# Optimization experiments

Measured on AMD Instinct MI355X. Metric: run time of the kernel, lower is better.

The kernel has to match this reference:

```python
import jax, jax.numpy as jnp
import numpy as np

DECAY = 0.9
BETA_OBS = 1.0
BETA_STATE = 1.0

N_OBS = 20000
N_STATES = 1024
N_ACTIONS = 64
STATE_DIM = 256
RFD = 2048


def setup_inputs() -> dict:
    key = jax.random.key(0)
    ks = jax.random.split(key, 7)
    Q = jax.random.normal(ks[0], (STATE_DIM, N_STATES), dtype=jnp.float32) / np.sqrt(STATE_DIM).astype(np.float32)
    V = jax.random.normal(ks[1], (STATE_DIM, N_ACTIONS), dtype=jnp.float32) / np.sqrt(STATE_DIM).astype(np.float32)
    W = jax.random.normal(ks[2], (RFD, STATE_DIM), dtype=jnp.float32)
    M_re = jax.random.normal(ks[3], (RFD, N_OBS), dtype=jnp.float32)
    M_im = jax.random.normal(ks[4], (RFD, N_OBS), dtype=jnp.float32)
    obs = jax.random.uniform(ks[5], (N_OBS,), dtype=jnp.float32)
    action = jax.random.uniform(ks[6], (N_ACTIONS,), dtype=jnp.float32)
    return {"Q": Q, "V": V, "W": W, "M_re": M_re, "M_im": M_im, "obs": obs, "action": action}


def reference(Q, V, W, M_re, M_im, obs, action):
    # One fused POCML step: memory write (decayed outer product), state
    # rotation via complex random-feature phase, clean_up (state-kernel
    # softmax retrieval), and obs retrieval from memory.
    D = W.shape[0]  # random_feature_dim
    M = M_re + 1j * M_im                       # [D, n_obs] complex64
    obs_c = obs.astype(jnp.complex64)
    # get_state_from_memory
    state0 = M @ obs_c                         # [D]
    # update_memory: M *= decay; M += outer(state, obs)
    M_new = DECAY * M + jnp.outer(state0, obs_c)
    # update_state: v = V @ action; phi_v = exp(1j * W @ v); state *= phi_v
    v = V @ action                             # [state_dim]
    phi_v = jnp.exp(1j * (W @ v))              # [D] complex64
    state1 = state0 * phi_v
    # clean_up: phi_Q = exp(1j * W @ Q), weights = softmax(beta*sim(phi_Q.T, state))
    phi_Q = jnp.exp(1j * (W @ Q))              # [D, n_states]
    score = BETA_STATE * (phi_Q.T @ jnp.conj(state1)).real / D  # [n_states]
    weights = jax.nn.softmax(score)
    state2 = phi_Q @ weights.astype(jnp.complex64)              # [D]
    # get_obs_from_memory: softmax(beta_obs * sim(M.T, state))
    obs_score = BETA_OBS * (M_new.T @ jnp.conj(state2)).real / D  # [n_obs]
    return jax.nn.softmax(obs_score)
```

## Files before the change

### kernel.cpp

```cpp
#include <hip/hip_runtime.h>
#include <math.h>

#define N_OBS    20000
#define N_OBS4   5000
#define N_STATES 1024
#define N_ACT    64
#define SDIM     256
#define RFD      2048
#define DECAY    0.9f

typedef float v4f __attribute__((ext_vector_type(4)));

__device__ __forceinline__ v4f ld4(const float* p) {
    return *(const v4f*)p;
}
__device__ __forceinline__ v4f ntload4(const float* p) {
    return __builtin_nontemporal_load((const v4f*)p);
}

#define OFF_SCORE  0
#define OFF_OBSACC 1024
#define ZERO_CNT   (OFF_OBSACC + N_OBS)
#define OFF_S0RE   21024
#define OFF_S0IM   23072
#define OFF_S2RE   25120
#define OFF_S2IM   27168
#define OFF_WTS    29216
#define OFF_VWS    30240
#define OFF_COSQ   30496
#define OFF_SINQ   (OFF_COSQ + RFD*N_STATES)
#define WS_FLOATS  (OFF_SINQ + RFD*N_STATES)

#define NB_GEMM   512
#define NB_P1     RFD
#define NB_FUSED  (NB_GEMM + 1 + NB_P1)

__global__ __launch_bounds__(256) void k_fused(
    const float* __restrict__ Mre, const float* __restrict__ Mim,
    const float* __restrict__ obs,
    const float* __restrict__ W, const float* __restrict__ Q,
    const float* __restrict__ V, const float* __restrict__ action,
    float* __restrict__ cosQ, float* __restrict__ sinQ,
    float* __restrict__ s0re, float* __restrict__ s0im,
    float* __restrict__ vout)
{
    const int b = blockIdx.x;
    const int tid = threadIdx.x;

    if (b < NB_GEMM) {
        __shared__ float As[16][65];
        __shared__ float Bs[16][64];
        const int tx = tid & 15;
        const int ty = tid >> 4;
        const int m0 = (b >> 4) * 64;
        const int n0 = (b & 15) * 64;
        float c[4][4] = {};
        for (int k0 = 0; k0 < SDIM; k0 += 16) {
            {
                int k = tid & 15, mb = tid >> 4;
                #pragma unroll
                for (int j = 0; j < 4; j++)
                    As[k][mb + 16*j] = W[(size_t)(m0 + mb + 16*j) * SDIM + k0 + k];
            }
            {
                int n = tid & 63, kb = tid >> 6;
                #pragma unroll
                for (int j = 0; j < 4; j++)
                    Bs[kb + 4*j][n] = Q[(size_t)(k0 + kb + 4*j) * N_STATES + n0 + n];
            }
            __syncthreads();
            #pragma unroll
            for (int kk = 0; kk < 16; kk++) {
                float a[4], bb[4];
                #pragma unroll
                for (int i = 0; i < 4; i++) a[i] = As[kk][ty*4 + i];
                #pragma unroll
                for (int j = 0; j < 4; j++) bb[j] = Bs[kk][tx*4 + j];
                #pragma unroll
                for (int i = 0; i < 4; i++)
                    #pragma unroll
                    for (int j = 0; j < 4; j++)
                        c[i][j] += a[i] * bb[j];
            }
            __syncthreads();
        }
        #pragma unroll
        for (int i = 0; i < 4; i++) {
            int d = m0 + ty*4 + i;
            #pragma unroll
            for (int j = 0; j < 4; j++) {
                int s = n0 + tx*4 + j;
                float sn, cs;
                sincosf(c[i][j], &sn, &cs);
                cosQ[(size_t)d * N_STATES + s] = cs;
                sinQ[(size_t)d * N_STATES + s] = sn;
            }
        }
    } else if (b == NB_GEMM) {
        float acc = 0.f;
        for (int a = 0; a < N_ACT; a++) acc += V[tid * N_ACT + a] * action[a];
        vout[tid] = acc;
    } else {
        const int d = b - (NB_GEMM + 1);
        const float* mr = Mre + (size_t)d * N_OBS;
        const float* mi = Mim + (size_t)d * N_OBS;
        const float4* ob = (const float4*)obs;
        float ar[4] = {0.f, 0.f, 0.f, 0.f}, ai[4] = {0.f, 0.f, 0.f, 0.f};
        int i = tid;
        #pragma unroll 4
        for (int it = 0; it < 19; ++it, i += 256) {
            float4 o = ob[i];
            v4f a = ld4(mr + 4 * (size_t)i);
            v4f m = ld4(mi + 4 * (size_t)i);
            ar[it & 3] += a.x*o.x + a.y*o.y + a.z*o.z + a.w*o.w;
            ai[it & 3] += m.x*o.x + m.y*o.y + m.z*o.z + m.w*o.w;
        }
        if (i < N_OBS4) {
            float4 o = ob[i];
            v4f a = ld4(mr + 4 * (size_t)i);
            v4f m = ld4(mi + 4 * (size_t)i);
            ar[3] += a.x*o.x + a.y*o.y + a.z*o.z + a.w*o.w;
            ai[3] += m.x*o.x + m.y*o.y + m.z*o.z + m.w*o.w;
        }
        float arr = (ar[0] + ar[1]) + (ar[2] + ar[3]);
        float aii = (ai[0] + ai[1]) + (ai[2] + ai[3]);
        #pragma unroll
        for (int off = 32; off > 0; off >>= 1) {
            arr += __shfl_down(arr, off);
            aii += __shfl_down(aii, off);
        }
        __shared__ float pr[4], pi[4];
        const int wave = tid >> 6, lane = tid & 63;
        if (lane == 0) { pr[wave] = arr; pi[wave] = aii; }
        __syncthreads();
        if (tid == 0) {
            s0re[d] = pr[0] + pr[1] + pr[2] + pr[3];
            s0im[d] = pi[0] + pi[1] + pi[2] + pi[3];
        }
    }
}

__global__ __launch_bounds__(256) void k_score(
    const float* __restrict__ cosQ, const float* __restrict__ sinQ,
    const float* __restrict__ W, const float* __restrict__ vws,
    const float* __restrict__ s0re, const float* __restrict__ s0im,
    float* __restrict__ score)
{
    __shared__ float s1r_s[32], s1i_s[32];
    const int tid = threadIdx.x;
    const int d0 = blockIdx.y * 32;
    {
        const int r = tid >> 3, g = tid & 7;
        const float4* wv4 = (const float4*)(W + (size_t)(d0 + r) * SDIM + g * 32);
        const float4* vv4 = (const float4*)(vws + g * 32);
        float th = 0.f;
        #pragma unroll
        for (int j = 0; j < 8; j++) {
            float4 wv = wv4[j], vv = vv4[j];
            th += wv.x*vv.x + wv.y*vv.y + wv.z*vv.z + wv.w*vv.w;
        }
        th += __shfl_xor(th, 4);
        th += __shfl_xor(th, 2);
        th += __shfl_xor(th, 1);
        if (g == 0) {
            float sn, cs;
            sincosf(th, &sn, &cs);
            float re = s0re[d0 + r], im = s0im[d0 + r];
            s1r_s[r] = re * cs - im * sn;
            s1i_s[r] = re * sn + im * cs;
        }
    }
    __syncthreads();
    const int s = blockIdx.x * 256 + tid;
    float acc = 0.f;
    #pragma unroll 4
    for (int j = 0; j < 32; j++) {
        int d = d0 + j;
        acc += cosQ[(size_t)d * N_STATES + s] * s1r_s[j]
             + sinQ[(size_t)d * N_STATES + s] * s1i_s[j];
    }
    atomicAdd(&score[s], acc);
}

__global__ __launch_bounds__(256) void k_softmax_w(
    const float* __restrict__ score, float* __restrict__ wts)
{
    __shared__ float red[256];
    const int tid = threadIdx.x;
    const float scale = 1.f / (float)RFD;
    float4 v = ((const float4*)score)[tid];
    v.x *= scale; v.y *= scale; v.z *= scale; v.w *= scale;
    float mx = fmaxf(fmaxf(v.x, v.y), fmaxf(v.z, v.w));
    red[tid] = mx; __syncthreads();
    for (int s = 128; s > 0; s >>= 1) {
        if (tid < s) red[tid] = fmaxf(red[tid], red[tid+s]);
        __syncthreads();
    }
    mx = red[0]; __syncthreads();
    float4 e;
    e.x = expf(v.x - mx); e.y = expf(v.y - mx);
    e.z = expf(v.z - mx); e.w = expf(v.w - mx);
    red[tid] = e.x + e.y + e.z + e.w; __syncthreads();
    for (int s = 128; s > 0; s >>= 1) {
        if (tid < s) red[tid] += red[tid+s];
        __syncthreads();
    }
    const float inv = 1.f / red[0];
    e.x *= inv; e.y *= inv; e.z *= inv; e.w *= inv;
    ((float4*)wts)[tid] = e;
}

__global__ __launch_bounds__(256) void k_state2(
    const float* __restrict__ cosQ, const float* __restrict__ sinQ,
    const float* __restrict__ wts,
    float* __restrict__ s2re, float* __restrict__ s2im)
{
    __shared__ float r1[256], r2[256];
    const int d = blockIdx.x, tid = threadIdx.x;
    float4 w = ((const float4*)wts)[tid];
    float4 a = ((const float4*)(cosQ + (size_t)d * N_STATES))[tid];
    float4 b = ((const float4*)(sinQ + (size_t)d * N_STATES))[tid];
    r1[tid] = a.x*w.x + a.y*w.y + a.z*w.z + a.w*w.w;
    r2[tid] = b.x*w.x + b.y*w.y + b.z*w.z + b.w*w.w;
    __syncthreads();
    for (int s = 128; s > 0; s >>= 1) {
        if (tid < s) { r1[tid] += r1[tid+s]; r2[tid] += r2[tid+s]; }
        __syncthreads();
    }
    if (tid == 0) { s2re[d] = r1[0]; s2im[d] = r2[0]; }
}

__global__ __launch_bounds__(256) void k_obs_acc(
    const float* __restrict__ Mre, const float* __restrict__ Mim,
    const float* __restrict__ s2re, const float* __restrict__ s2im,
    float* __restrict__ obs_acc)
{
    __shared__ float c_s[64], s_s[64];
    const int tid = threadIdx.x;
    const int dbase = (31 - (int)blockIdx.y) * 64;
    if (tid < 64) { c_s[tid] = s2re[dbase + tid]; s_s[tid] = s2im[dbase + tid]; }
    __syncthreads();
    const int idx = blockIdx.x * 256 + tid;
    if (idx >= N_OBS4) return;
    float4 acc[4];
    #pragma unroll
    for (int u = 0; u < 4; u++) acc[u] = make_float4(0.f, 0.f, 0.f, 0.f);
    #pragma unroll 8
    for (int j = 0; j < 64; j++) {
        size_t base = ((size_t)(dbase + j) * N_OBS4 + idx) * 4;
        v4f a = ntload4(Mre + base);
        v4f b = ntload4(Mim + base);
        float cc = c_s[j], ss = s_s[j];
        acc[j & 3].x += a.x*cc + b.x*ss;
        acc[j & 3].y += a.y*cc + b.y*ss;
        acc[j & 3].z += a.z*cc + b.z*ss;
        acc[j & 3].w += a.w*cc + b.w*ss;
    }
    float4 t;
    t.x = (acc[0].x + acc[1].x) + (acc[2].x + acc[3].x);
    t.y = (acc[0].y + acc[1].y) + (acc[2].y + acc[3].y);
    t.z = (acc[0].z + acc[1].z) + (acc[2].z + acc[3].z);
    t.w = (acc[0].w + acc[1].w) + (acc[2].w + acc[3].w);
    atomicAdd(&obs_acc[idx*4 + 0], t.x);
    atomicAdd(&obs_acc[idx*4 + 1], t.y);
    atomicAdd(&obs_acc[idx*4 + 2], t.z);
    atomicAdd(&obs_acc[idx*4 + 3], t.w);
}

__global__ __launch_bounds__(1024) void k_softmax_obs(
    const float* __restrict__ obs_acc, const float* __restrict__ obs,
    const float* __restrict__ s0re, const float* __restrict__ s0im,
    const float* __restrict__ s2re, const float* __restrict__ s2im,
    float* __restrict__ out)
{
    __shared__ float red[1024];
    const int tid = threadIdx.x;
    float dp = 0.f;
    #pragma unroll
    for (int i = 0; i < 2; i++) {
        int d = tid + i * 1024;
        dp += s0re[d] * s2re[d] + s0im[d] * s2im[d];
    }
    red[tid] = dp; __syncthreads();
    for (int s = 512; s > 0; s >>= 1) {
        if (tid < s) red[tid] += red[tid+s];
        __syncthreads();
    }
    const float d0 = red[0];
    __syncthreads();
    const float scale = 1.f / (float)RFD;
    float vals[20];
    float mx = -3.402823466e+38f;
    #pragma unroll
    for (int i = 0; i < 20; i++) {
        int idx = tid + i * 1024;
        if (idx < N_OBS) {
            float sc = (DECAY * obs_acc[idx] + obs[idx] * d0) * scale;
            vals[i] = sc;
            mx = fmaxf(mx, sc);
        } else vals[i] = -3.402823466e+38f;
    }
    red[tid] = mx; __syncthreads();
    for (int s = 512; s > 0; s >>= 1) {
        if (tid < s) red[tid] = fmaxf(red[tid], red[tid+s]);
        __syncthreads();
    }
    mx = red[0]; __syncthreads();
    float sum = 0.f;
    #pragma unroll
    for (int i = 0; i < 20; i++) {
        int idx = tid + i * 1024;
        if (idx < N_OBS) {
            vals[i] = expf(vals[i] - mx);
            sum += vals[i];
        }
    }
    red[tid] = sum; __syncthreads();
    for (int s = 512; s > 0; s >>= 1) {
        if (tid < s) red[tid] += red[tid+s];
        __syncthreads();
    }
    const float inv = 1.f / red[0];
    #pragma unroll
    for (int i = 0; i < 20; i++) {
        int idx = tid + i * 1024;
        if (idx < N_OBS) out[idx] = vals[i] * inv;
    }
}

extern "C" void kernel_launch(void* const* d_in, const int* in_sizes, int n_in,
                              void* d_out, int out_size, void* d_ws, size_t ws_size,
                              hipStream_t stream) {
    const float* Q      = (const float*)d_in[0];
    const float* V      = (const float*)d_in[1];
    const float* W      = (const float*)d_in[2];
    const float* Mre    = (const float*)d_in[3];
    const float* Mim    = (const float*)d_in[4];
    const float* obs    = (const float*)d_in[5];
    const float* action = (const float*)d_in[6];
    float* out = (float*)d_out;
    float* ws  = (float*)d_ws;

    if (ws_size < (size_t)WS_FLOATS * sizeof(float)) return;

    float* score = ws + OFF_SCORE;
    float* oacc  = ws + OFF_OBSACC;
    float* s0re  = ws + OFF_S0RE;
    float* s0im  = ws + OFF_S0IM;
    float* s2re  = ws + OFF_S2RE;
    float* s2im  = ws + OFF_S2IM;
    float* wts   = ws + OFF_WTS;
    float* vws   = ws + OFF_VWS;
    float* cosQ  = ws + OFF_COSQ;
    float* sinQ  = ws + OFF_SINQ;

    hipMemsetAsync(ws, 0, (size_t)ZERO_CNT * sizeof(float), stream);

    k_fused<<<NB_FUSED, 256, 0, stream>>>(Mre, Mim, obs, W, Q, V, action,
                                          cosQ, sinQ, s0re, s0im, vws);
    k_score<<<dim3(4, 64), 256, 0, stream>>>(cosQ, sinQ, W, vws, s0re, s0im, score);
    k_softmax_w<<<1, 256, 0, stream>>>(score, wts);
    k_state2<<<RFD, 256, 0, stream>>>(cosQ, sinQ, wts, s2re, s2im);
    k_obs_acc<<<dim3(20, 32), 256, 0, stream>>>(Mre, Mim, s2re, s2im, oacc);
    k_softmax_obs<<<1, 1024, 0, stream>>>(oacc, obs, s0re, s0im, s2re, s2im, out);
}
```

Before: 421.8 us.

## Stash fp16 interleaved copy of memory matrix for second pass

During the first pass over M_re/M_im (computing state0), blocks now handle two rows each and also write an interleaved fp16 copy of M into workspace. The later obs-score pass reads this half-size copy instead of re-reading both fp32 matrices, halving its traffic. The cost is extra write traffic in the first pass, fp16 rounding of M in the obs scores, and reliance on a much larger workspace, with a fallback to the fp32 path when the workspace is too small. Block ordering in the fused kernel and the obs pass is also changed.

```diff
diff --git a/kernel.cpp b/kernel.cpp
--- a/kernel.cpp
+++ b/kernel.cpp
@@ -1,4 +1,5 @@
 #include <hip/hip_runtime.h>
+#include <hip/hip_fp16.h>
 #include <math.h>
 
 #define N_OBS    20000
@@ -16,6 +17,15 @@
 }
 __device__ __forceinline__ v4f ntload4(const float* p) {
     return __builtin_nontemporal_load((const v4f*)p);
+}
+
+__device__ __forceinline__ uint4 pack8(v4f re, v4f im) {
+    union { __half h[8]; uint4 u; } p;
+    p.h[0] = __float2half_rn(re.x); p.h[1] = __float2half_rn(im.x);
+    p.h[2] = __float2half_rn(re.y); p.h[3] = __float2half_rn(im.y);
+    p.h[4] = __float2half_rn(re.z); p.h[5] = __float2half_rn(im.z);
+    p.h[6] = __float2half_rn(re.w); p.h[7] = __float2half_rn(im.w);
+    return p.u;
 }
 
 #define OFF_SCORE  0
@@ -29,11 +39,14 @@
 #define OFF_VWS    30240
 #define OFF_COSQ   30496
 #define OFF_SINQ   (OFF_COSQ + RFD*N_STATES)
-#define WS_FLOATS  (OFF_SINQ + RFD*N_STATES)
-
+#define OFF_MH     (OFF_SINQ + RFD*N_STATES)
+#define MH_FLOATS  (RFD * N_OBS4 * 4)
+#define WS_BASE_FLOATS (OFF_MH)
+#define WS_FP16_FLOATS (OFF_MH + MH_FLOATS)
+
+#define NB_P1     (RFD / 2)
 #define NB_GEMM   512
-#define NB_P1     RFD
-#define NB_FUSED  (NB_GEMM + 1 + NB_P1)
+#define NB_FUSED  (NB_P1 + 1 + NB_GEMM)
 
 __global__ __launch_bounds__(256) void k_fused(
     const float* __restrict__ Mre, const float* __restrict__ Mim,
@@ -42,18 +55,116 @@
     const float* __restrict__ V, const float* __restrict__ action,
     float* __restrict__ cosQ, float* __restrict__ sinQ,
     float* __restrict__ s0re, float* __restrict__ s0im,
-    float* __restrict__ vout)
+    float* __restrict__ vout, uint4* __restrict__ Mh, int writeMh)
 {
     const int b = blockIdx.x;
     const int tid = threadIdx.x;
 
-    if (b < NB_GEMM) {
+    if (b < NB_P1) {
+        const int d0 = b * 2;
+        const float* mr0 = Mre + (size_t)d0 * N_OBS;
+        const float* mi0 = Mim + (size_t)d0 * N_OBS;
+        const float* mr1 = mr0 + N_OBS;
+        const float* mi1 = mi0 + N_OBS;
+        uint4* mh0 = Mh + (size_t)d0 * N_OBS4;
+        uint4* mh1 = mh0 + N_OBS4;
+        const float4* ob = (const float4*)obs;
+        float a0r[2] = {0.f, 0.f}, a0i[2] = {0.f, 0.f};
+        float a1r[2] = {0.f, 0.f}, a1i[2] = {0.f, 0.f};
+        int i = tid;
+        if (writeMh) {
+            #pragma unroll 2
+            for (int it = 0; it < 19; ++it, i += 256) {
+                float4 o = ob[i];
+                v4f r0 = ntload4(mr0 + 4 * (size_t)i);
+                v4f q0 = ntload4(mi0 + 4 * (size_t)i);
+                v4f r1 = ntload4(mr1 + 4 * (size_t)i);
+                v4f q1 = ntload4(mi1 + 4 * (size_t)i);
+                mh0[i] = pack8(r0, q0);
+                mh1[i] = pack8(r1, q1);
+                a0r[it & 1] += r0.x*o.x + r0.y*o.y + r0.z*o.z + r0.w*o.w;
+                a0i[it & 1] += q0.x*o.x + q0.y*o.y + q0.z*o.z + q0.w*o.w;
+                a1r[it & 1] += r1.x*o.x + r1.y*o.y + r1.z*o.z + r1.w*o.w;
+                a1i[it & 1] += q1.x*o.x + q1.y*o.y + q1.z*o.z + q1.w*o.w;
+            }
+            if (i < N_OBS4) {
+                float4 o = ob[i];
+                v4f r0 = ntload4(mr0 + 4 * (size_t)i);
+                v4f q0 = ntload4(mi0 + 4 * (size_t)i);
+                v4f r1 = ntload4(mr1 + 4 * (size_t)i);
+                v4f q1 = ntload4(mi1 + 4 * (size_t)i);
+                mh0[i] = pack8(r0, q0);
+                mh1[i] = pack8(r1, q1);
+                a0r[0] += r0.x*o.x + r0.y*o.y + r0.z*o.z + r0.w*o.w;
+                a0i[0] += q0.x*o.x + q0.y*o.y + q0.z*o.z + q0.w*o.w;
+                a1r[0] += r1.x*o.x + r1.y*o.y + r1.z*o.z + r1.w*o.w;
+                a1i[0] += q1.x*o.x + q1.y*o.y + q1.z*o.z + q1.w*o.w;
+            }
+        } else {
+            #pragma unroll 2
+            for (int it = 0; it < 19; ++it, i += 256) {
+                float4 o = ob[i];
+                v4f r0 = ntload4(mr0 + 4 * (size_t)i);
+                v4f q0 = ntload4(mi0 + 4 * (size_t)i);
+                v4f r1 = ntload4(mr1 + 4 * (size_t)i);
+                v4f q1 = ntload4(mi1 + 4 * (size_t)i);
+                a0r[it & 1] += r0.x*o.x + r0.y*o.y + r0.z*o.z + r0.w*o.w;
+                a0i[it & 1] += q0.x*o.x + q0.y*o.y + q0.z*o.z + q0.w*o.w;
+                a1r[it & 1] += r1.x*o.x + r1.y*o.y + r1.z*o.z + r1.w*o.w;
+                a1i[it & 1] += q1.x*o.x + q1.y*o.y + q1.z*o.z + q1.w*o.w;
+            }
+            if (i < N_OBS4) {
+                float4 o = ob[i];
+                v4f r0 = ntload4(mr0 + 4 * (size_t)i);
+                v4f q0 = ntload4(mi0 + 4 * (size_t)i);
+                v4f r1 = ntload4(mr1 + 4 * (size_t)i);
+                v4f q1 = ntload4(mi1 + 4 * (size_t)i);
+                a0r[0] += r0.x*o.x + r0.y*o.y + r0.z*o.z + r0.w*o.w;
+                a0i[0] += q0.x*o.x + q0.y*o.y + q0.z*o.z + q0.w*o.w;
+                a1r[0] += r1.x*o.x + r1.y*o.y + r1.z*o.z + r1.w*o.w;
+                a1i[0] += q1.x*o.x + q1.y*o.y + q1.z*o.z + q1.w*o.w;
+            }
+        }
+        float v0 = a0r[0] + a0r[1];
+        float v1 = a0i[0] + a0i[1];
+        float v2 = a1r[0] + a1r[1];
+        float v3 = a1i[0] + a1i[1];
+        #pragma unroll
+        for (int off = 32; off > 0; off >>= 1) {
+            v0 += __shfl_down(v0, off);
+            v1 += __shfl_down(v1, off);
+            v2 += __shfl_down(v2, off);
+            v3 += __shfl_down(v3, off);
+        }
+        __shared__ float red[4][4];
+        const int wave = tid >> 6, lane = tid & 63;
+        if (lane == 0) {
+            red[wave][0] = v0; red[wave][1] = v1;
+            red[wave][2] = v2; red[wave][3] = v3;
+        }
+        __syncthreads();
+        if (tid == 0) {
+            float r0 = 0.f, i0 = 0.f, r1 = 0.f, i1 = 0.f;
+            #pragma unroll
+            for (int w = 0; w < 4; w++) {
+                r0 += red[w][0]; i0 += red[w][1];
+                r1 += red[w][2]; i1 += red[w][3];
+            }
+            s0re[d0] = r0; s0im[d0] = i0;
+            s0re[d0 + 1] = r1; s0im[d0 + 1] = i1;
+        }
+    } else if (b == NB_P1) {
+        float acc = 0.f;
+        for (int a = 0; a < N_ACT; a++) acc += V[tid * N_ACT + a] * action[a];
+        vout[tid] = acc;
+    } else {
+        const int g = b - (NB_P1 + 1);
         __shared__ float As[16][65];
         __shared__ float Bs[16][64];
         const int tx = tid & 15;
         const int ty = tid >> 4;
-        const int m0 = (b >> 4) * 64;
-        const int n0 = (b & 15) * 64;
+        const int m0 = (g >> 4) * 64;
+        const int n0 = (g & 15) * 64;
         float c[4][4] = {};
         for (int k0 = 0; k0 < SDIM; k0 += 16) {
             {
@@ -96,47 +207,6 @@
                 sinQ[(size_t)d * N_STATES + s] = sn;
             }
         }
-    } else if (b == NB_GEMM) {
-        float acc = 0.f;
-        for (int a = 0; a < N_ACT; a++) acc += V[tid * N_ACT + a] * action[a];
-        vout[tid] = acc;
-    } else {
-        const int d = b - (NB_GEMM + 1);
-        const float* mr = Mre + (size_t)d * N_OBS;
-        const float* mi = Mim + (size_t)d * N_OBS;
-        const float4* ob = (const float4*)obs;
-        float ar[4] = {0.f, 0.f, 0.f, 0.f}, ai[4] = {0.f, 0.f, 0.f, 0.f};
-        int i = tid;
-        #pragma unroll 4
-        for (int it = 0; it < 19; ++it, i += 256) {
-            float4 o = ob[i];
-            v4f a = ld4(mr + 4 * (size_t)i);
-            v4f m = ld4(mi + 4 * (size_t)i);
-            ar[it & 3] += a.x*o.x + a.y*o.y + a.z*o.z + a.w*o.w;
-            ai[it & 3] += m.x*o.x + m.y*o.y + m.z*o.z + m.w*o.w;
-        }
-        if (i < N_OBS4) {
-            float4 o = ob[i];
-            v4f a = ld4(mr + 4 * (size_t)i);
-            v4f m = ld4(mi + 4 * (size_t)i);
-            ar[3] += a.x*o.x + a.y*o.y + a.z*o.z + a.w*o.w;
-            ai[3] += m.x*o.x + m.y*o.y + m.z*o.z + m.w*o.w;
-        }
-        float arr = (ar[0] + ar[1]) + (ar[2] + ar[3]);
-        float aii = (ai[0] + ai[1]) + (ai[2] + ai[3]);
-        #pragma unroll
-        for (int off = 32; off > 0; off >>= 1) {
-            arr += __shfl_down(arr, off);
-            aii += __shfl_down(aii, off);
-        }
-        __shared__ float pr[4], pi[4];
-        const int wave = tid >> 6, lane = tid & 63;
-        if (lane == 0) { pr[wave] = arr; pi[wave] = aii; }
-        __syncthreads();
-        if (tid == 0) {
-            s0re[d] = pr[0] + pr[1] + pr[2] + pr[3];
-            s0im[d] = pi[0] + pi[1] + pi[2] + pi[3];
-        }
     }
 }
 
@@ -230,14 +300,56 @@
     if (tid == 0) { s2re[d] = r1[0]; s2im[d] = r2[0]; }
 }
 
-__global__ __launch_bounds__(256) void k_obs_acc(
+__global__ __launch_bounds__(256) void k_obs_acc_h(
+    const uint4* __restrict__ Mh,
+    const float* __restrict__ s2re, const float* __restrict__ s2im,
+    float* __restrict__ obs_acc)
+{
+    __shared__ float c_s[64], s_s[64];
+    const int tid = threadIdx.x;
+    const int dbase = blockIdx.y * 64;
+    if (tid < 64) { c_s[tid] = s2re[dbase + tid]; s_s[tid] = s2im[dbase + tid]; }
+    __syncthreads();
+    const int idx = blockIdx.x * 256 + tid;
+    if (idx >= N_OBS4) return;
+    const uint4* p = Mh + (size_t)dbase * N_OBS4 + idx;
+    float4 acc[4];
+    #pragma unroll
+    for (int u = 0; u < 4; u++) acc[u] = make_float4(0.f, 0.f, 0.f, 0.f);
+    #pragma unroll 8
+    for (int j = 0; j < 64; ++j) {
+        uint4 u = p[(size_t)j * N_OBS4];
+        float cc = c_s[j], ss = s_s[j];
+        union { unsigned u; __half2 h; } w0, w1, w2, w3;
+        w0.u = u.x; w1.u = u.y; w2.u = u.z; w3.u = u.w;
+        float2 f0 = __half22float2(w0.h);
+        float2 f1 = __half22float2(w1.h);
+        float2 f2 = __half22float2(w2.h);
+        float2 f3 = __half22float2(w3.h);
+        acc[j & 3].x += f0.x*cc + f0.y*ss;
+        acc[j & 3].y += f1.x*cc + f1.y*ss;
+        acc[j & 3].z += f2.x*cc + f2.y*ss;
+        acc[j & 3].w += f3.x*cc + f3.y*ss;
+    }
+    float4 t;
+    t.x = (acc[0].x + acc[1].x) + (acc[2].x + acc[3].x);
+    t.y = (acc[0].y + acc[1].y) + (acc[2].y + acc[3].y);
+    t.z = (acc[0].z + acc[1].z) + (acc[2].z + acc[3].z);
+    t.w = (acc[0].w + acc[1].w) + (acc[2].w + acc[3].w);
+    atomicAdd(&obs_acc[idx*4 + 0], t.x);
+    atomicAdd(&obs_acc[idx*4 + 1], t.y);
+    atomicAdd(&obs_acc[idx*4 + 2], t.z);
+    atomicAdd(&obs_acc[idx*4 + 3], t.w);
+}
+
+__global__ __launch_bounds__(256) void k_obs_acc_f32(
     const float* __restrict__ Mre, const float* __restrict__ Mim,
     const float* __restrict__ s2re, const float* __restrict__ s2im,
     float* __restrict__ obs_acc)
 {
     __shared__ float c_s[64], s_s[64];
     const int tid = threadIdx.x;
-    const int dbase = (31 - (int)blockIdx.y) * 64;
+    const int dbase = blockIdx.y * 64;
     if (tid < 64) { c_s[tid] = s2re[dbase + tid]; s_s[tid] = s2im[dbase + tid]; }
     __syncthreads();
     const int idx = blockIdx.x * 256 + tid;
@@ -341,7 +453,8 @@
     float* out = (float*)d_out;
     float* ws  = (float*)d_ws;
 
-    if (ws_size < (size_t)WS_FLOATS * sizeof(float)) return;
+    if (ws_size < (size_t)WS_BASE_FLOATS * sizeof(float)) return;
+    const int fp16path = ws_size >= (size_t)WS_FP16_FLOATS * sizeof(float);
 
     float* score = ws + OFF_SCORE;
     float* oacc  = ws + OFF_OBSACC;
@@ -353,14 +466,19 @@
     float* vws   = ws + OFF_VWS;
     float* cosQ  = ws + OFF_COSQ;
     float* sinQ  = ws + OFF_SINQ;
+    uint4* Mh    = (uint4*)(ws + OFF_MH);
 
     hipMemsetAsync(ws, 0, (size_t)ZERO_CNT * sizeof(float), stream);
 
     k_fused<<<NB_FUSED, 256, 0, stream>>>(Mre, Mim, obs, W, Q, V, action,
-                                          cosQ, sinQ, s0re, s0im, vws);
+                                          cosQ, sinQ, s0re, s0im, vws,
+                                          Mh, fp16path);
     k_score<<<dim3(4, 64), 256, 0, stream>>>(cosQ, sinQ, W, vws, s0re, s0im, score);
     k_softmax_w<<<1, 256, 0, stream>>>(score, wts);
     k_state2<<<RFD, 256, 0, stream>>>(cosQ, sinQ, wts, s2re, s2im);
-    k_obs_acc<<<dim3(20, 32), 256, 0, stream>>>(Mre, Mim, s2re, s2im, oacc);
+    if (fp16path)
+        k_obs_acc_h<<<dim3(20, 32), 256, 0, stream>>>(Mh, s2re, s2im, oacc);
+    else
+        k_obs_acc_f32<<<dim3(20, 32), 256, 0, stream>>>(Mre, Mim, s2re, s2im, oacc);
     k_softmax_obs<<<1, 1024, 0, stream>>>(oacc, obs, s0re, s0im, s2re, s2im, out);
 }
```

After: 414.8 us. Within noise of the previous version (-1.7%).

## Cache interleaved FP8 copy of M during first pass for obs retrieval

Applied to the files above, without the earlier changes.

The first pass over M_re/M_im now also writes an interleaved FP8 copy of the memory matrix to workspace, and the final obs-score GEMV reads that copy instead of re-reading both fp32 matrices. This is meant to cut the second full pass's memory traffic roughly fourfold. The first pass is also split into five segments per row to expose more parallelism, with the partial sums reduced downstream. The cost is an extra write stream and FP8 quantization error in the obs scores, which may fail accuracy tolerance.

```diff
diff --git a/kernel.cpp b/kernel.cpp
--- a/kernel.cpp
+++ b/kernel.cpp
@@ -3,37 +3,46 @@
 
 #define N_OBS    20000
 #define N_OBS4   5000
+#define N_OBS8   2500
 #define N_STATES 1024
 #define N_ACT    64
 #define SDIM     256
 #define RFD      2048
 #define DECAY    0.9f
+#define NSEG     5
+#define SEG_O8   500
 
 typedef float v4f __attribute__((ext_vector_type(4)));
-
-__device__ __forceinline__ v4f ld4(const float* p) {
-    return *(const v4f*)p;
-}
+typedef float v2f __attribute__((ext_vector_type(2)));
+
 __device__ __forceinline__ v4f ntload4(const float* p) {
     return __builtin_nontemporal_load((const v4f*)p);
+}
+
+__device__ __forceinline__ unsigned pk4_fp8(float a, float b, float c, float d) {
+    unsigned w = __builtin_amdgcn_cvt_pk_fp8_f32(a, b, 0u, false);
+    w = __builtin_amdgcn_cvt_pk_fp8_f32(c, d, w, true);
+    return w;
 }
 
 #define OFF_SCORE  0
 #define OFF_OBSACC 1024
 #define ZERO_CNT   (OFF_OBSACC + N_OBS)
-#define OFF_S0RE   21024
-#define OFF_S0IM   23072
-#define OFF_S2RE   25120
-#define OFF_S2IM   27168
-#define OFF_WTS    29216
-#define OFF_VWS    30240
-#define OFF_COSQ   30496
+#define OFF_P0RE   21024
+#define OFF_P0IM   (OFF_P0RE + NSEG*RFD)
+#define OFF_S2RE   (OFF_P0IM + NSEG*RFD)
+#define OFF_S2IM   (OFF_S2RE + RFD)
+#define OFF_WTS    (OFF_S2IM + RFD)
+#define OFF_VWS    (OFF_WTS + N_STATES)
+#define OFF_COSQ   (OFF_VWS + SDIM)
 #define OFF_SINQ   (OFF_COSQ + RFD*N_STATES)
-#define WS_FLOATS  (OFF_SINQ + RFD*N_STATES)
-
+#define OFF_MH8    (OFF_SINQ + RFD*N_STATES)
+#define MH8_FLOATS (RFD * N_OBS8 * 4)
+#define WS_FLOATS  (OFF_MH8 + MH8_FLOATS)
+
+#define NB_P1     (RFD * NSEG)
 #define NB_GEMM   512
-#define NB_P1     RFD
-#define NB_FUSED  (NB_GEMM + 1 + NB_P1)
+#define NB_FUSED  (NB_P1 + 1 + NB_GEMM)
 
 __global__ __launch_bounds__(256) void k_fused(
     const float* __restrict__ Mre, const float* __restrict__ Mim,
@@ -41,19 +50,84 @@
     const float* __restrict__ W, const float* __restrict__ Q,
     const float* __restrict__ V, const float* __restrict__ action,
     float* __restrict__ cosQ, float* __restrict__ sinQ,
-    float* __restrict__ s0re, float* __restrict__ s0im,
-    float* __restrict__ vout)
+    float* __restrict__ p0re, float* __restrict__ p0im,
+    float* __restrict__ vout, uint4* __restrict__ Mh8)
 {
     const int b = blockIdx.x;
     const int tid = threadIdx.x;
 
-    if (b < NB_GEMM) {
+    if (b < NB_P1) {
+        const int d = b / NSEG;
+        const int seg = b - d * NSEG;
+        const float* mr = Mre + (size_t)d * N_OBS;
+        const float* mi = Mim + (size_t)d * N_OBS;
+        uint4* mh = Mh8 + (size_t)d * N_OBS8;
+        const float4* ob = (const float4*)obs;
+        const int i0 = seg * SEG_O8;
+        float ar0 = 0.f, ai0 = 0.f, ar1 = 0.f, ai1 = 0.f;
+        {
+            int i = i0 + tid;
+            float4 oa = ob[2*i], obv = ob[2*i + 1];
+            v4f ra = ntload4(mr + 8 * (size_t)i);
+            v4f rb = ntload4(mr + 8 * (size_t)i + 4);
+            v4f qa = ntload4(mi + 8 * (size_t)i);
+            v4f qb = ntload4(mi + 8 * (size_t)i + 4);
+            uint4 u;
+            u.x = pk4_fp8(ra.x, qa.x, ra.y, qa.y);
+            u.y = pk4_fp8(ra.z, qa.z, ra.w, qa.w);
+            u.z = pk4_fp8(rb.x, qb.x, rb.y, qb.y);
+            u.w = pk4_fp8(rb.z, qb.z, rb.w, qb.w);
+            mh[i] = u;
+            ar0 += ra.x*oa.x + ra.y*oa.y + ra.z*oa.z + ra.w*oa.w;
+            ar1 += rb.x*obv.x + rb.y*obv.y + rb.z*obv.z + rb.w*obv.w;
+            ai0 += qa.x*oa.x + qa.y*oa.y + qa.z*oa.z + qa.w*oa.w;
+            ai1 += qb.x*obv.x + qb.y*obv.y + qb.z*obv.z + qb.w*obv.w;
+        }
+        if (tid < SEG_O8 - 256) {
+            int i = i0 + 256 + tid;
+            float4 oa = ob[2*i], obv = ob[2*i + 1];
+            v4f ra = ntload4(mr + 8 * (size_t)i);
+            v4f rb = ntload4(mr + 8 * (size_t)i + 4);
+            v4f qa = ntload4(mi + 8 * (size_t)i);
+            v4f qb = ntload4(mi + 8 * (size_t)i + 4);
+            uint4 u;
+            u.x = pk4_fp8(ra.x, qa.x, ra.y, qa.y);
+            u.y = pk4_fp8(ra.z, qa.z, ra.w, qa.w);
+            u.z = pk4_fp8(rb.x, qb.x, rb.y, qb.y);
+            u.w = pk4_fp8(rb.z, qb.z, rb.w, qb.w);
+            mh[i] = u;
+            ar0 += ra.x*oa.x + ra.y*oa.y + ra.z*oa.z + ra.w*oa.w;
+            ar1 += rb.x*obv.x + rb.y*obv.y + rb.z*obv.z + rb.w*obv.w;
+            ai0 += qa.x*oa.x + qa.y*oa.y + qa.z*oa.z + qa.w*oa.w;
+            ai1 += qb.x*obv.x + qb.y*obv.y + qb.z*obv.z + qb.w*obv.w;
+        }
+        float arr = ar0 + ar1;
+        float aii = ai0 + ai1;
+        #pragma unroll
+        for (int off = 32; off > 0; off >>= 1) {
+            arr += __shfl_down(arr, off);
+            aii += __shfl_down(aii, off);
+        }
+        __shared__ float pr[4], pi[4];
+        const int wave = tid >> 6, lane = tid & 63;
+        if (lane == 0) { pr[wave] = arr; pi[wave] = aii; }
+        __syncthreads();
+        if (tid == 0) {
+            p0re[seg * RFD + d] = pr[0] + pr[1] + pr[2] + pr[3];
+            p0im[seg * RFD + d] = pi[0] + pi[1] + pi[2] + pi[3];
+        }
+    } else if (b == NB_P1) {
+        float acc = 0.f;
+        for (int a = 0; a < N_ACT; a++) acc += V[tid * N_ACT + a] * action[a];
+        vout[tid] = acc;
+    } else {
+        const int g = b - (NB_P1 + 1);
         __shared__ float As[16][65];
         __shared__ float Bs[16][64];
         const int tx = tid & 15;
         const int ty = tid >> 4;
-        const int m0 = (b >> 4) * 64;
-        const int n0 = (b & 15) * 64;
+        const int m0 = (g >> 4) * 64;
+        const int n0 = (g & 15) * 64;
         float c[4][4] = {};
         for (int k0 = 0; k0 < SDIM; k0 += 16) {
             {
@@ -96,54 +170,13 @@
                 sinQ[(size_t)d * N_STATES + s] = sn;
             }
         }
-    } else if (b == NB_GEMM) {
-        float acc = 0.f;
-        for (int a = 0; a < N_ACT; a++) acc += V[tid * N_ACT + a] * action[a];
-        vout[tid] = acc;
-    } else {
-        const int d = b - (NB_GEMM + 1);
-        const float* mr = Mre + (size_t)d * N_OBS;
-        const float* mi = Mim + (size_t)d * N_OBS;
-        const float4* ob = (const float4*)obs;
-        float ar[4] = {0.f, 0.f, 0.f, 0.f}, ai[4] = {0.f, 0.f, 0.f, 0.f};
-        int i = tid;
-        #pragma unroll 4
-        for (int it = 0; it < 19; ++it, i += 256) {
-            float4 o = ob[i];
-            v4f a = ld4(mr + 4 * (size_t)i);
-            v4f m = ld4(mi + 4 * (size_t)i);
-            ar[it & 3] += a.x*o.x + a.y*o.y + a.z*o.z + a.w*o.w;
-            ai[it & 3] += m.x*o.x + m.y*o.y + m.z*o.z + m.w*o.w;
-        }
-        if (i < N_OBS4) {
-            float4 o = ob[i];
-            v4f a = ld4(mr + 4 * (size_t)i);
-            v4f m = ld4(mi + 4 * (size_t)i);
-            ar[3] += a.x*o.x + a.y*o.y + a.z*o.z + a.w*o.w;
-            ai[3] += m.x*o.x + m.y*o.y + m.z*o.z + m.w*o.w;
-        }
-        float arr = (ar[0] + ar[1]) + (ar[2] + ar[3]);
-        float aii = (ai[0] + ai[1]) + (ai[2] + ai[3]);
-        #pragma unroll
-        for (int off = 32; off > 0; off >>= 1) {
-            arr += __shfl_down(arr, off);
-            aii += __shfl_down(aii, off);
-        }
-        __shared__ float pr[4], pi[4];
-        const int wave = tid >> 6, lane = tid & 63;
-        if (lane == 0) { pr[wave] = arr; pi[wave] = aii; }
-        __syncthreads();
-        if (tid == 0) {
-            s0re[d] = pr[0] + pr[1] + pr[2] + pr[3];
-            s0im[d] = pi[0] + pi[1] + pi[2] + pi[3];
-        }
     }
 }
 
 __global__ __launch_bounds__(256) void k_score(
     const float* __restrict__ cosQ, const float* __restrict__ sinQ,
     const float* __restrict__ W, const float* __restrict__ vws,
-    const float* __restrict__ s0re, const float* __restrict__ s0im,
+    const float* __restrict__ p0re, const float* __restrict__ p0im,
     float* __restrict__ score)
 {
     __shared__ float s1r_s[32], s1i_s[32];
@@ -163,9 +196,15 @@
         th += __shfl_xor(th, 2);
         th += __shfl_xor(th, 1);
         if (g == 0) {
+            const int d = d0 + r;
+            float re = 0.f, im = 0.f;
+            #pragma unroll
+            for (int s = 0; s < NSEG; s++) {
+                re += p0re[s * RFD + d];
+                im += p0im[s * RFD + d];
+            }
             float sn, cs;
             sincosf(th, &sn, &cs);
-            float re = s0re[d0 + r], im = s0im[d0 + r];
             s1r_s[r] = re * cs - im * sn;
             s1i_s[r] = re * sn + im * cs;
         }
@@ -230,46 +269,56 @@
     if (tid == 0) { s2re[d] = r1[0]; s2im[d] = r2[0]; }
 }
 
-__global__ __launch_bounds__(256) void k_obs_acc(
-    const float* __restrict__ Mre, const float* __restrict__ Mim,
+__global__ __launch_bounds__(256) void k_obs_acc8(
+    const uint4* __restrict__ Mh8,
     const float* __restrict__ s2re, const float* __restrict__ s2im,
     float* __restrict__ obs_acc)
 {
-    __shared__ float c_s[64], s_s[64];
+    __shared__ float c_s[32], s_s[32];
     const int tid = threadIdx.x;
-    const int dbase = (31 - (int)blockIdx.y) * 64;
-    if (tid < 64) { c_s[tid] = s2re[dbase + tid]; s_s[tid] = s2im[dbase + tid]; }
+    const int dbase = blockIdx.y * 32;
+    if (tid < 32) { c_s[tid] = s2re[dbase + tid]; s_s[tid] = s2im[dbase + tid]; }
     __syncthreads();
     const int idx = blockIdx.x * 256 + tid;
-    if (idx >= N_OBS4) return;
-    float4 acc[4];
-    #pragma unroll
-    for (int u = 0; u < 4; u++) acc[u] = make_float4(0.f, 0.f, 0.f, 0.f);
-    #pragma unroll 8
-    for (int j = 0; j < 64; j++) {
-        size_t base = ((size_t)(dbase + j) * N_OBS4 + idx) * 4;
-        v4f a = ntload4(Mre + base);
-        v4f b = ntload4(Mim + base);
+    if (idx >= N_OBS8) return;
+    const uint4* p = Mh8 + (size_t)dbase * N_OBS8 + idx;
+    float a0 = 0.f, a1 = 0.f, a2 = 0.f, a3 = 0.f;
+    float a4 = 0.f, a5 = 0.f, a6 = 0.f, a7 = 0.f;
+    #pragma unroll 4
+    for (int j = 0; j < 32; ++j) {
+        uint4 u = p[(size_t)j * N_OBS8];
         float cc = c_s[j], ss = s_s[j];
-        acc[j & 3].x += a.x*cc + b.x*ss;
-        acc[j & 3].y += a.y*cc + b.y*ss;
-        acc[j & 3].z += a.z*cc + b.z*ss;
-        acc[j & 3].w += a.w*cc + b.w*ss;
-    }
-    float4 t;
-    t.x = (acc[0].x + acc[1].x) + (acc[2].x + acc[3].x);
-    t.y = (acc[0].y + acc[1].y) + (acc[2].y + acc[3].y);
-    t.z = (acc[0].z + acc[1].z) + (acc[2].z + acc[3].z);
-    t.w = (acc[0].w + acc[1].w) + (acc[2].w + acc[3].w);
-    atomicAdd(&obs_acc[idx*4 + 0], t.x);
-    atomicAdd(&obs_acc[idx*4 + 1], t.y);
-    atomicAdd(&obs_acc[idx*4 + 2], t.z);
-    atomicAdd(&obs_acc[idx*4 + 3], t.w);
+        v2f f0 = __builtin_amdgcn_cvt_pk_f32_fp8(u.x, false);
+        v2f f1 = __builtin_amdgcn_cvt_pk_f32_fp8(u.x, true);
+        v2f f2 = __builtin_amdgcn_cvt_pk_f32_fp8(u.y, false);
+        v2f f3 = __builtin_amdgcn_cvt_pk_f32_fp8(u.y, true);
+        v2f f4 = __builtin_amdgcn_cvt_pk_f32_fp8(u.z, false);
+        v2f f5 = __builtin_amdgcn_cvt_pk_f32_fp8(u.z, true);
+        v2f f6 = __builtin_amdgcn_cvt_pk_f32_fp8(u.w, false);
+        v2f f7 = __builtin_amdgcn_cvt_pk_f32_fp8(u.w, true);
+        a0 += f0.x*cc + f0.y*ss;
+        a1 += f1.x*cc + f1.y*ss;
+        a2 += f2.x*cc + f2.y*ss;
+        a3 += f3.x*cc + f3.y*ss;
+        a4 += f4.x*cc + f4.y*ss;
+        a5 += f5.x*cc + f5.y*ss;
+        a6 += f6.x*cc + f6.y*ss;
+        a7 += f7.x*cc + f7.y*ss;
+    }
+    float* dst = obs_acc + idx * 8;
+    atomicAdd(dst + 0, a0);
+    atomicAdd(dst + 1, a1);
+    atomicAdd(dst + 2, a2);
+    atomicAdd(dst + 3, a3);
+    atomicAdd(dst + 4, a4);
+    atomicAdd(dst + 5, a5);
+    atomicAdd(dst + 6, a6);
+    atomicAdd(dst + 7, a7);
 }
 
 __global__ __launch_bounds__(1024) void k_softmax_obs(
     const float* __restrict__ obs_acc, const float* __restrict__ obs,
-    const float* __restrict__ s0re, const float* __restrict__ s0im,
+    const float* __restrict__ p0re, const float* __restrict__ p0im,
     const float* __restrict__ s2re, const float* __restrict__ s2im,
     float* __restrict__ out)
 {
@@ -279,7 +328,13 @@
     #pragma unroll
     for (int i = 0; i < 2; i++) {
         int d = tid + i * 1024;
-        dp += s0re[d] * s2re[d] + s0im[d] * s2im[d];
+        float re = 0.f, im = 0.f;
+        #pragma unroll
+        for (int s = 0; s < NSEG; s++) {
+            re += p0re[s * RFD + d];
+            im += p0im[s * RFD + d];
+        }
+        dp += re * s2re[d] + im * s2im[d];
     }
     red[tid] = dp; __syncthreads();
     for (int s = 512; s > 0; s >>= 1) {
@@ -345,22 +400,23 @@
 
     float* score = ws + OFF_SCORE;
     float* oacc  = ws + OFF_OBSACC;
-    float* s0re  = ws + OFF_S0RE;
-    float* s0im  = ws + OFF_S0IM;
+    float* p0re  = ws + OFF_P0RE;
+    float* p0im  = ws + OFF_P0IM;
     float* s2re  = ws + OFF_S2RE;
     float* s2im  = ws + OFF_S2IM;
     float* wts   = ws + OFF_WTS;
     float* vws   = ws + OFF_VWS;
     float* cosQ  = ws + OFF_COSQ;
     float* sinQ  = ws + OFF_SINQ;
+    uint4* Mh8   = (uint4*)(ws + OFF_MH8);
 
     hipMemsetAsync(ws, 0, (size_t)ZERO_CNT * sizeof(float), stream);
 
     k_fused<<<NB_FUSED, 256, 0, stream>>>(Mre, Mim, obs, W, Q, V, action,
-                                          cosQ, sinQ, s0re, s0im, vws);
-    k_score<<<dim3(4, 64), 256, 0, stream>>>(cosQ, sinQ, W, vws, s0re, s0im, score);
+                                          cosQ, sinQ, p0re, p0im, vws, Mh8);
+    k_score<<<dim3(4, 64), 256, 0, stream>>>(cosQ, sinQ, W, vws, p0re, p0im, score);
     k_softmax_w<<<1, 256, 0, stream>>>(score, wts);
     k_state2<<<RFD, 256, 0, stream>>>(cosQ, sinQ, wts, s2re, s2im);
-    k_obs_acc<<<dim3(20, 32), 256, 0, stream>>>(Mre, Mim, s2re, s2im, oacc);
-    k_softmax_obs<<<1, 1024, 0, stream>>>(oacc, obs, s0re, s0im, s2re, s2im, out);
-}
+    k_obs_acc8<<<dim3(10, 64), 256, 0, stream>>>(Mh8, s2re, s2im, oacc);
+    k_softmax_obs<<<1, 1024, 0, stream>>>(oacc, obs, p0re, p0im, s2re, s2im, out);
+}
```

Result: slower. 444.4 us (+5.4%).

## Stage M as interleaved fp16 during first pass and read it in obs accumulation

Applied to the files above, without the earlier changes.

While computing M·obs, the first pass now also writes M_re and M_im as an interleaved half-precision copy in the workspace. The final obs-score reduction reads that copy instead of re-reading both fp32 matrices, which halves the bytes of the second pass and may let them stay in the last-level cache. The first pass is split into two half-row blocks with partial sums combined downstream, and the memset is replaced by zeroing blocks inside the fused kernel. In exchange the first pass gains a large write stream, and the obs scores lose accuracy from rounding M to fp16.

```diff
diff --git a/kernel.cpp b/kernel.cpp
--- a/kernel.cpp
+++ b/kernel.cpp
@@ -1,4 +1,5 @@
 #include <hip/hip_runtime.h>
+#include <hip/hip_fp16.h>
 #include <math.h>
 
 #define N_OBS    20000
@@ -8,32 +9,43 @@
 #define SDIM     256
 #define RFD      2048
 #define DECAY    0.9f
+#define HALF_O8  1250
+#define FLTMAX   3.402823466e+38f
 
 typedef float v4f __attribute__((ext_vector_type(4)));
 
-__device__ __forceinline__ v4f ld4(const float* p) {
-    return *(const v4f*)p;
-}
 __device__ __forceinline__ v4f ntload4(const float* p) {
     return __builtin_nontemporal_load((const v4f*)p);
 }
 
+__device__ __forceinline__ uint4 pack8(v4f re, v4f im) {
+    union { __half h[8]; uint4 u; } p;
+    p.h[0] = __float2half_rn(re.x); p.h[1] = __float2half_rn(im.x);
+    p.h[2] = __float2half_rn(re.y); p.h[3] = __float2half_rn(im.y);
+    p.h[4] = __float2half_rn(re.z); p.h[5] = __float2half_rn(im.z);
+    p.h[6] = __float2half_rn(re.w); p.h[7] = __float2half_rn(im.w);
+    return p.u;
+}
+
 #define OFF_SCORE  0
 #define OFF_OBSACC 1024
-#define ZERO_CNT   (OFF_OBSACC + N_OBS)
-#define OFF_S0RE   21024
-#define OFF_S0IM   23072
-#define OFF_S2RE   25120
-#define OFF_S2IM   27168
-#define OFF_WTS    29216
-#define OFF_VWS    30240
-#define OFF_COSQ   30496
+#define ZERO_CNT   21024
+#define OFF_P0RE   21024
+#define OFF_P0IM   (OFF_P0RE + 2*RFD)
+#define OFF_S2RE   (OFF_P0IM + 2*RFD)
+#define OFF_S2IM   (OFF_S2RE + RFD)
+#define OFF_WTS    (OFF_S2IM + RFD)
+#define OFF_VWS    (OFF_WTS + N_STATES)
+#define OFF_COSQ   (OFF_VWS + SDIM)
 #define OFF_SINQ   (OFF_COSQ + RFD*N_STATES)
-#define WS_FLOATS  (OFF_SINQ + RFD*N_STATES)
+#define OFF_MH     (OFF_SINQ + RFD*N_STATES)
+#define MH_FLOATS  (RFD * N_OBS4 * 4)
+#define WS_FLOATS  (OFF_MH + MH_FLOATS)
 
 #define NB_GEMM   512
-#define NB_P1     RFD
-#define NB_FUSED  (NB_GEMM + 1 + NB_P1)
+#define NB_Z      21
+#define NB_P1     (RFD * 2)
+#define NB_FUSED  (NB_GEMM + 1 + NB_Z + NB_P1)
 
 __global__ __launch_bounds__(256) void k_fused(
     const float* __restrict__ Mre, const float* __restrict__ Mim,
@@ -41,8 +53,9 @@
     const float* __restrict__ W, const float* __restrict__ Q,
     const float* __restrict__ V, const float* __restrict__ action,
     float* __restrict__ cosQ, float* __restrict__ sinQ,
-    float* __restrict__ s0re, float* __restrict__ s0im,
-    float* __restrict__ vout)
+    float* __restrict__ p0re, float* __restrict__ p0im,
+    float* __restrict__ vout, uint4* __restrict__ Mh,
+    float* __restrict__ zbase)
 {
     const int b = blockIdx.x;
     const int tid = threadIdx.x;
@@ -100,30 +113,40 @@
         float acc = 0.f;
         for (int a = 0; a < N_ACT; a++) acc += V[tid * N_ACT + a] * action[a];
         vout[tid] = acc;
+    } else if (b < NB_GEMM + 1 + NB_Z) {
+        int idx = (b - (NB_GEMM + 1)) * 256 + tid;
+        if (idx < ZERO_CNT / 4)
+            ((float4*)zbase)[idx] = make_float4(0.f, 0.f, 0.f, 0.f);
     } else {
-        const int d = b - (NB_GEMM + 1);
+        const int p = b - (NB_GEMM + 1 + NB_Z);
+        const int d = p >> 1;
+        const int h = p & 1;
         const float* mr = Mre + (size_t)d * N_OBS;
         const float* mi = Mim + (size_t)d * N_OBS;
+        uint4* mh = Mh + (size_t)d * N_OBS4;
         const float4* ob = (const float4*)obs;
-        float ar[4] = {0.f, 0.f, 0.f, 0.f}, ai[4] = {0.f, 0.f, 0.f, 0.f};
-        int i = tid;
-        #pragma unroll 4
-        for (int it = 0; it < 19; ++it, i += 256) {
-            float4 o = ob[i];
-            v4f a = ld4(mr + 4 * (size_t)i);
-            v4f m = ld4(mi + 4 * (size_t)i);
-            ar[it & 3] += a.x*o.x + a.y*o.y + a.z*o.z + a.w*o.w;
-            ai[it & 3] += m.x*o.x + m.y*o.y + m.z*o.z + m.w*o.w;
-        }
-        if (i < N_OBS4) {
-            float4 o = ob[i];
-            v4f a = ld4(mr + 4 * (size_t)i);
-            v4f m = ld4(mi + 4 * (size_t)i);
-            ar[3] += a.x*o.x + a.y*o.y + a.z*o.z + a.w*o.w;
-            ai[3] += m.x*o.x + m.y*o.y + m.z*o.z + m.w*o.w;
-        }
-        float arr = (ar[0] + ar[1]) + (ar[2] + ar[3]);
-        float aii = (ai[0] + ai[1]) + (ai[2] + ai[3]);
+        const int base = h * HALF_O8, lim = base + HALF_O8;
+        float ar0 = 0.f, ar1 = 0.f, ai0 = 0.f, ai1 = 0.f;
+        int i = base + tid;
+        #pragma unroll
+        for (int it = 0; it < 5; ++it, i += 256) {
+            int ic = i < lim ? i : lim - 1;
+            float4 oa = ob[2*ic], obv = ob[2*ic + 1];
+            v4f ra = ntload4(mr + 8 * (size_t)ic);
+            v4f rb = ntload4(mr + 8 * (size_t)ic + 4);
+            v4f qa = ntload4(mi + 8 * (size_t)ic);
+            v4f qb = ntload4(mi + 8 * (size_t)ic + 4);
+            if (i < lim) {
+                mh[2*ic]     = pack8(ra, qa);
+                mh[2*ic + 1] = pack8(rb, qb);
+                ar0 += ra.x*oa.x + ra.y*oa.y + ra.z*oa.z + ra.w*oa.w;
+                ar1 += rb.x*obv.x + rb.y*obv.y + rb.z*obv.z + rb.w*obv.w;
+                ai0 += qa.x*oa.x + qa.y*oa.y + qa.z*oa.z + qa.w*oa.w;
+                ai1 += qb.x*obv.x + qb.y*obv.y + qb.z*obv.z + qb.w*obv.w;
+            }
+        }
+        float arr = ar0 + ar1;
+        float aii = ai0 + ai1;
         #pragma unroll
         for (int off = 32; off > 0; off >>= 1) {
             arr += __shfl_down(arr, off);
@@ -134,8 +157,8 @@
         if (lane == 0) { pr[wave] = arr; pi[wave] = aii; }
         __syncthreads();
         if (tid == 0) {
-            s0re[d] = pr[0] + pr[1] + pr[2] + pr[3];
-            s0im[d] = pi[0] + pi[1] + pi[2] + pi[3];
+            p0re[h * RFD + d] = pr[0] + pr[1] + pr[2] + pr[3];
+            p0im[h * RFD + d] = pi[0] + pi[1] + pi[2] + pi[3];
         }
     }
 }
@@ -143,7 +166,7 @@
 __global__ __launch_bounds__(256) void k_score(
     const float* __restrict__ cosQ, const float* __restrict__ sinQ,
     const float* __restrict__ W, const float* __restrict__ vws,
-    const float* __restrict__ s0re, const float* __restrict__ s0im,
+    const float* __restrict__ p0re, const float* __restrict__ p0im,
     float* __restrict__ score)
 {
     __shared__ float s1r_s[32], s1i_s[32];
@@ -163,9 +186,11 @@
         th += __shfl_xor(th, 2);
         th += __shfl_xor(th, 1);
         if (g == 0) {
+            const int d = d0 + r;
+            float re = p0re[d] + p0re[RFD + d];
+            float im = p0im[d] + p0im[RFD + d];
             float sn, cs;
             sincosf(th, &sn, &cs);
-            float re = s0re[d0 + r], im = s0im[d0 + r];
             s1r_s[r] = re * cs - im * sn;
             s1i_s[r] = re * sn + im * cs;
         }
@@ -230,8 +255,8 @@
     if (tid == 0) { s2re[d] = r1[0]; s2im[d] = r2[0]; }
 }
 
-__global__ __launch_bounds__(256) void k_obs_acc(
-    const float* __restrict__ Mre, const float* __restrict__ Mim,
+__global__ __launch_bounds__(256) void k_obs_acc_h(
+    const uint4* __restrict__ Mh,
     const float* __restrict__ s2re, const float* __restrict__ s2im,
     float* __restrict__ obs_acc)
 {
@@ -242,19 +267,24 @@
     __syncthreads();
     const int idx = blockIdx.x * 256 + tid;
     if (idx >= N_OBS4) return;
+    const uint4* p = Mh + (size_t)dbase * N_OBS4 + idx;
     float4 acc[4];
     #pragma unroll
     for (int u = 0; u < 4; u++) acc[u] = make_float4(0.f, 0.f, 0.f, 0.f);
     #pragma unroll 8
-    for (int j = 0; j < 64; j++) {
-        size_t base = ((size_t)(dbase + j) * N_OBS4 + idx) * 4;
-        v4f a = ntload4(Mre + base);
-        v4f b = ntload4(Mim + base);
+    for (int j = 0; j < 64; ++j) {
+        uint4 u = p[(size_t)j * N_OBS4];
         float cc = c_s[j], ss = s_s[j];
-        acc[j & 3].x += a.x*cc + b.x*ss;
-        acc[j & 3].y += a.y*cc + b.y*ss;
-        acc[j & 3].z += a.z*cc + b.z*ss;
-        acc[j & 3].w += a.w*cc + b.w*ss;
+        union { unsigned u; __half2 h; } w0, w1, w2, w3;
+        w0.u = u.x; w1.u = u.y; w2.u = u.z; w3.u = u.w;
+        float2 f0 = __half22float2(w0.h);
+        float2 f1 = __half22float2(w1.h);
+        float2 f2 = __half22float2(w2.h);
+        float2 f3 = __half22float2(w3.h);
+        acc[j & 3].x += f0.x*cc + f0.y*ss;
+        acc[j & 3].y += f1.x*cc + f1.y*ss;
+        acc[j & 3].z += f2.x*cc + f2.y*ss;
+        acc[j & 3].w += f3.x*cc + f3.y*ss;
     }
     float4 t;
     t.x = (acc[0].x + acc[1].x) + (acc[2].x + acc[3].x);
@@ -269,7 +299,7 @@
 
 __global__ __launch_bounds__(1024) void k_softmax_obs(
     const float* __restrict__ obs_acc, const float* __restrict__ obs,
-    const float* __restrict__ s0re, const float* __restrict__ s0im,
+    const float* __restrict__ p0re, const float* __restrict__ p0im,
     const float* __restrict__ s2re, const float* __restrict__ s2im,
     float* __restrict__ out)
 {
@@ -279,7 +309,9 @@
     #pragma unroll
     for (int i = 0; i < 2; i++) {
         int d = tid + i * 1024;
-        dp += s0re[d] * s2re[d] + s0im[d] * s2im[d];
+        float re = p0re[d] + p0re[RFD + d];
+        float im = p0im[d] + p0im[RFD + d];
+        dp += re * s2re[d] + im * s2im[d];
     }
     red[tid] = dp; __syncthreads();
     for (int s = 512; s > 0; s >>= 1) {
@@ -290,7 +322,7 @@
     __syncthreads();
     const float scale = 1.f / (float)RFD;
     float vals[20];
-    float mx = -3.402823466e+38f;
+    float mx = -FLTMAX;
     #pragma unroll
     for (int i = 0; i < 20; i++) {
         int idx = tid + i * 1024;
@@ -298,7 +330,7 @@
             float sc = (DECAY * obs_acc[idx] + obs[idx] * d0) * scale;
             vals[i] = sc;
             mx = fmaxf(mx, sc);
-        } else vals[i] = -3.402823466e+38f;
+        } else vals[i] = -FLTMAX;
     }
     red[tid] = mx; __syncthreads();
     for (int s = 512; s > 0; s >>= 1) {
@@ -345,22 +377,21 @@
 
     float* score = ws + OFF_SCORE;
     float* oacc  = ws + OFF_OBSACC;
-    float* s0re  = ws + OFF_S0RE;
-    float* s0im  = ws + OFF_S0IM;
+    float* p0re  = ws + OFF_P0RE;
+    float* p0im  = ws + OFF_P0IM;
     float* s2re  = ws + OFF_S2RE;
     float* s2im  = ws + OFF_S2IM;
     float* wts   = ws + OFF_WTS;
     float* vws   = ws + OFF_VWS;
     float* cosQ  = ws + OFF_COSQ;
     float* sinQ  = ws + OFF_SINQ;
-
-    hipMemsetAsync(ws, 0, (size_t)ZERO_CNT * sizeof(float), stream);
+    uint4* Mh    = (uint4*)(ws + OFF_MH);
 
     k_fused<<<NB_FUSED, 256, 0, stream>>>(Mre, Mim, obs, W, Q, V, action,
-                                          cosQ, sinQ, s0re, s0im, vws);
-    k_score<<<dim3(4, 64), 256, 0, stream>>>(cosQ, sinQ, W, vws, s0re, s0im, score);
+                                          cosQ, sinQ, p0re, p0im, vws, Mh, ws);
+    k_score<<<dim3(4, 64), 256, 0, stream>>>(cosQ, sinQ, W, vws, p0re, p0im, score);
     k_softmax_w<<<1, 256, 0, stream>>>(score, wts);
     k_state2<<<RFD, 256, 0, stream>>>(cosQ, sinQ, wts, s2re, s2im);
-    k_obs_acc<<<dim3(20, 32), 256, 0, stream>>>(Mre, Mim, s2re, s2im, oacc);
-    k_softmax_obs<<<1, 1024, 0, stream>>>(oacc, obs, s0re, s0im, s2re, s2im, out);
-}
+    k_obs_acc_h<<<dim3(20, 32), 256, 0, stream>>>(Mh, s2re, s2im, oacc);
+    k_softmax_obs<<<1, 1024, 0, stream>>>(oacc, obs, p0re, p0im, s2re, s2im, out);
+}
```

After: 424.0 us. No clear change (+0.5%).
